# Kernel tuning notes

Hardware: AMD Instinct MI355X
Metric: run time of the kernel (lower is better)

Reference implementation:

```python
import jax, jax.numpy as jnp
import numpy as np

V, S, D, H, DK, DV, DFF, L, B, PAD = 32000, 2048, 512, 8, 64, 64, 2048, 2, 2, 0


def _pos_encoding(s, d):
    pos = jnp.arange(s, dtype=jnp.float32)[:, None]
    idx = jnp.arange(d // 2, dtype=jnp.float32)
    ang = pos / (10000.0 ** (2.0 * idx / d))  # [s, d/2]
    pe = jnp.zeros((s, d), jnp.float32)
    pe = pe.at[:, 0::2].set(jnp.sin(ang))
    pe = pe.at[:, 1::2].set(jnp.cos(ang))
    return pe


def _stable_softmax(x):
    # matches torch: max clamped to >= 0, denom + 1e-9 (all -inf row -> zeros)
    m = jnp.clip(jnp.max(x, axis=-1, keepdims=True), 0.0, None)
    e = jnp.exp(x - m)
    return e / (jnp.sum(e, axis=-1, keepdims=True) + 1e-9)


def _ln(x, s, b):
    mu = jnp.mean(x, axis=-1, keepdims=True)
    var = jnp.mean((x - mu) ** 2, axis=-1, keepdims=True)
    return (x - mu) / jnp.sqrt(var + 1e-5) * s + b


def setup_inputs() -> dict:
    key = jax.random.key(0)
    ks = jax.random.split(key, 16)
    sc = 0.02
    emb = sc * jax.random.normal(ks[1], (V, D), jnp.float32)
    emb = emb.at[PAD].set(0.0)  # padding_idx row is zero
    return {
        'x': jax.random.randint(ks[0], (B, S), 0, V),
        'padding_mask': jnp.zeros((B, S), bool),
        'emb': emb,
        'wq': sc * jax.random.normal(ks[2], (L, D, H * DK), jnp.float32),
        'wk': sc * jax.random.normal(ks[3], (L, D, H * DK), jnp.float32),
        'wv': sc * jax.random.normal(ks[4], (L, D, H * DV), jnp.float32),
        'wo': sc * jax.random.normal(ks[5], (L, H * DV, D), jnp.float32),
        'ln1_s': jnp.ones((L, D), jnp.float32),
        'ln1_b': jnp.zeros((L, D), jnp.float32),
        'ln2_s': jnp.ones((L, D), jnp.float32),
        'ln2_b': jnp.zeros((L, D), jnp.float32),
        'w1': sc * jax.random.normal(ks[6], (L, D, DFF), jnp.float32),
        'b1': jnp.zeros((L, DFF), jnp.float32),
        'w2': sc * jax.random.normal(ks[7], (L, DFF, D), jnp.float32),
        'b2': jnp.zeros((L, D), jnp.float32),
        'w_out': sc * jax.random.normal(ks[8], (D, V), jnp.float32),
    }


def _forward(x, padding_mask, emb, wq, wk, wv, wo, ln1_s, ln1_b, ln2_s, ln2_b, w1, b1, w2, b2, w_out):
    b, s = x.shape
    pe = _pos_encoding(s, D)[None]  # [1, s, D]
    pe = jnp.where(padding_mask[:, :, None], 0.0, pe)  # zero PE at padding tokens
    h = emb[x] + pe  # [b, s, D]
    # causal mask INCLUDES the diagonal (torch.triu default), union with padding rows/cols
    causal = jnp.triu(jnp.ones((s, s), bool))
    mask = causal[None, None] | padding_mask[:, None, None, :] | padding_mask[:, None, :, None]
    for l in range(L):
        q = (h @ wq[l]).reshape(b, s, H, DK).transpose(0, 2, 1, 3)
        k = (h @ wk[l]).reshape(b, s, H, DK).transpose(0, 2, 1, 3)
        v = (h @ wv[l]).reshape(b, s, H, DV).transpose(0, 2, 1, 3)
        scores = jnp.einsum('bhqd,bhkd->bhqk', q, k) / jnp.sqrt(jnp.float32(DK))
        scores = jnp.where(mask, -jnp.inf, scores)
        attn = _stable_softmax(scores)  # [b, H, s, s]
        o = jnp.einsum('bhqk,bhkd->bhqd', attn, v)
        o = o.transpose(0, 2, 1, 3).reshape(b, s, H * DV) @ wo[l]
        h = _ln(h + o, ln1_s[l], ln1_b[l])  # post-LN residual
        ff = jax.nn.gelu(h @ w1[l] + b1[l], approximate=False) @ w2[l] + b2[l]
        h = _ln(h + ff, ln2_s[l], ln2_b[l])
    return h @ w_out  # logits [b, s, V]


def reference(x, padding_mask, emb, wq, wk, wv, wo, ln1_s, ln1_b, ln2_s, ln2_b, w1, b1, w2, b2, w_out):
    return _forward(x, padding_mask, emb, wq, wk, wv, wo, ln1_s, ln1_b, ln2_s, ln2_b, w1, b1, w2, b2, w_out)
```

## Files before the change

kernel.cpp:

```cpp
#include <hip/hip_runtime.h>
#include <hip/hip_bf16.h>
#include <stdint.h>

#define VOCAB  32000
#define SLEN   2048
#define DMODEL 512
#define NHEAD  8
#define HDIM   64
#define DFFN   2048
#define NLAYER 2
#define BATCH  2
#define NTOK   (BATCH*SLEN)

typedef unsigned short u16;
using short8 = __attribute__((ext_vector_type(8))) short;
using f32x4  = __attribute__((ext_vector_type(4))) float;
using ushort4v = __attribute__((ext_vector_type(4))) unsigned short;

__device__ __forceinline__ u16 f2bf(float f) {
  union { float f; uint32_t i; } v; v.f = f;
  uint32_t r = v.i + 0x7fffu + ((v.i >> 16) & 1u);
  return (u16)(r >> 16);
}

__device__ __forceinline__ void gload_lds16(const void* g, void* l) {
  __builtin_amdgcn_global_load_lds(
      (const __attribute__((address_space(1))) unsigned int*)g,
      (__attribute__((address_space(3))) unsigned int*)l,
      16, 0, 0);
}

__device__ __forceinline__ void tr_tile(const float* __restrict__ in, u16* __restrict__ out,
                                        int K, int N, int nb, int kb, int tid) {
  __shared__ float t[32][33];
  int tx = tid & 31, ty = tid >> 5;
  #pragma unroll
  for (int i = 0; i < 32; i += 8)
    t[ty + i][tx] = in[(size_t)(kb + ty + i) * N + nb + tx];
  __syncthreads();
  #pragma unroll
  for (int i = 0; i < 32; i += 8)
    out[(size_t)(nb + ty + i) * K + kb + tx] = f2bf(t[tx][ty + i]);
}

__global__ void transpose_qkvo(const float* __restrict__ wq, const float* __restrict__ wk,
                               const float* __restrict__ wv, const float* __restrict__ wo,
                               u16* __restrict__ qkvT, u16* __restrict__ woT) {
  int job = blockIdx.y;
  int l = job >> 2, which = job & 3;
  const float* in = (which == 0) ? wq : (which == 1) ? wk : (which == 2) ? wv : wo;
  in += (size_t)l * DMODEL * DMODEL;
  u16* out = (which < 3) ? qkvT + (size_t)l * 1536 * DMODEL + (size_t)which * DMODEL * DMODEL
                         : woT + (size_t)l * DMODEL * DMODEL;
  int tile = blockIdx.x;
  tr_tile(in, out, DMODEL, DMODEL, (tile & 15) * 32, (tile >> 4) * 32, threadIdx.x);
}

__global__ void transpose_ffn(const float* __restrict__ w1, const float* __restrict__ w2,
                              u16* __restrict__ w1T, u16* __restrict__ w2T) {
  int job = blockIdx.y;
  int l = job >> 1, which = job & 1;
  const float* in;
  u16* out;
  int K, N;
  if (which == 0) { in = w1 + (size_t)l * DMODEL * DFFN; out = w1T + (size_t)l * DFFN * DMODEL; K = DMODEL; N = DFFN; }
  else            { in = w2 + (size_t)l * DFFN * DMODEL; out = w2T + (size_t)l * DMODEL * DFFN; K = DFFN; N = DMODEL; }
  int tile = blockIdx.x;
  int ntx = N / 32;
  tr_tile(in, out, K, N, (tile % ntx) * 32, (tile / ntx) * 32, threadIdx.x);
}

__global__ void transpose_wout_kmaj(const float* __restrict__ in, u16* __restrict__ out) {
  const int nb = blockIdx.x, kt = blockIdx.y;
  const int t = threadIdx.x;
  u16* dst = out + ((size_t)(nb * 8 + kt)) * 16384;
  #pragma unroll
  for (int kg = 0; kg < 8; ++kg) {
    short8 v;
    #pragma unroll
    for (int e = 0; e < 8; ++e)
      v[e] = (short)f2bf(in[(size_t)(kt * 64 + kg * 8 + e) * VOCAB + nb * 256 + t]);
    *(short8*)(dst + (kg * 256 + t) * 8) = v;
  }
}

__global__ void embed_pe(const int* __restrict__ x, const float* __restrict__ emb,
                         float* __restrict__ hf, u16* __restrict__ hb) {
  int tok = blockIdx.x;
  int s = tok & (SLEN - 1);
  int d = threadIdx.x << 2;
  int t = x[tok];
  float4 ev = *(const float4*)(emb + (size_t)t * DMODEL + d);
  float pos = (float)s;
  const float cexp = -0.03597789207803197f;
  float i0 = (float)(d >> 1);
  float a0 = pos * expf(cexp * i0);
  float a1 = pos * expf(cexp * (i0 + 1.0f));
  float h0 = ev.x + sinf(a0);
  float h1 = ev.y + cosf(a0);
  float h2 = ev.z + sinf(a1);
  float h3 = ev.w + cosf(a1);
  size_t o = (size_t)tok * DMODEL + d;
  *(float4*)(hf + o) = make_float4(h0, h1, h2, h3);
  hb[o + 0] = f2bf(h0); hb[o + 1] = f2bf(h1);
  hb[o + 2] = f2bf(h2); hb[o + 3] = f2bf(h3);
}

template<int EPI, bool XCDS, int BM, int BN>
__global__ __launch_bounds__(256, 2)
void gemm_nt(const u16* __restrict__ A, const u16* __restrict__ Bt,
             float* __restrict__ Cf, u16* __restrict__ Cb, u16* __restrict__ Vt,
             const float* __restrict__ bias, int M, int N, int K) {
  constexpr int MI = BM / 32;
  constexpr int NI = BN / 32;
  __shared__ u16 As[BM * 64];
  __shared__ u16 Bs[BN * 64];
  const int tid = threadIdx.x;
  const int lane = tid & 63;
  const int lr = lane & 15, lg = lane >> 4;
  const int w = tid >> 6;

  int bx = blockIdx.x, by = blockIdx.y;
  if constexpr (XCDS) {
    int nwg = gridDim.x * gridDim.y;
    int bid = by * gridDim.x + bx;
    int cpx = nwg >> 3;
    bid = (bid & 7) * cpx + (bid >> 3);
    bx = bid % gridDim.x; by = bid / gridDim.x;
  }
  const int m0 = by * BM;
  const int n0 = bx * BN;
  const int wm = (w >> 1) * (BM / 2);
  const int wn = (w & 1) * (BN / 2);

  f32x4 acc[MI][NI] = {};

  for (int kt = 0; kt < K; kt += 64) {
    #pragma unroll
    for (int r = 0; r < BM / 32; ++r) {
      int chunk = r * 256 + tid;
      int row = chunk >> 3, ce = (chunk & 7) * 8;
      gload_lds16(A + (size_t)(m0 + row) * K + kt + ce, As + chunk * 8);
    }
    #pragma unroll
    for (int r = 0; r < BN / 32; ++r) {
      int chunk = r * 256 + tid;
      int row = chunk >> 3, ce = (chunk & 7) * 8;
      gload_lds16(Bt + (size_t)(n0 + row) * K + kt + ce, Bs + chunk * 8);
    }
    __syncthreads();
    #pragma unroll
    for (int ks = 0; ks < 2; ++ks) {
      short8 af[MI], bfr[NI];
      #pragma unroll
      for (int mi = 0; mi < MI; ++mi)
        af[mi] = *(const short8*)(As + (wm + mi * 16 + lr) * 64 + ks * 32 + lg * 8);
      #pragma unroll
      for (int ni = 0; ni < NI; ++ni)
        bfr[ni] = *(const short8*)(Bs + (wn + ni * 16 + lr) * 64 + ks * 32 + lg * 8);
      #pragma unroll
      for (int mi = 0; mi < MI; ++mi)
        #pragma unroll
        for (int ni = 0; ni < NI; ++ni)
          acc[mi][ni] = __builtin_amdgcn_mfma_f32_16x16x32_bf16(af[mi], bfr[ni], acc[mi][ni], 0, 0, 0);
    }
    __syncthreads();
  }

  #pragma unroll
  for (int mi = 0; mi < MI; ++mi)
    #pragma unroll
    for (int ni = 0; ni < NI; ++ni) {
      const int col = n0 + wn + ni * 16 + lr;
      const int row0 = m0 + wm + mi * 16 + lg * 4;
      float bv = 0.f;
      if constexpr (EPI == 3) bv = bias[col];
      if constexpr (EPI == 2) {
        if (col >= 1024) {
          int hd = col - 1024, hh = hd >> 6, d = hd & 63;
          int b2 = row0 >> 11, s = row0 & (SLEN - 1);
          int c2 = (s >> 3) & 15, e2 = s & 7;
          int cs2 = c2 ^ (d & 7);
          ushort4v pk;
          #pragma unroll
          for (int j = 0; j < 4; ++j) pk[j] = f2bf(acc[mi][ni][j]);
          size_t va = ((size_t)((b2 * NHEAD + hh) * HDIM + d) << 11) + (s & ~127) + cs2 * 8 + e2;
          *(ushort4v*)(Vt + va) = pk;
          continue;
        }
      }
      #pragma unroll
      for (int j = 0; j < 4; ++j) {
        const int row = row0 + j;
        float v = acc[mi][ni][j];
        if constexpr (EPI == 0) {
          Cf[(size_t)row * N + col] = v;
        } else if constexpr (EPI == 2) {
          int dh = col & 63;
          int cs = (col & ~63) | ((((dh >> 3) ^ (row & 7)) << 3) | (dh & 7));
          Cb[(size_t)row * N + cs] = f2bf(v);
        } else {
          float xb = v + bv;
          Cb[(size_t)row * N + col] = f2bf(0.5f * xb * (1.0f + erff(xb * 0.7071067811865476f)));
        }
      }
    }
}

template<int EPI, bool XCDS>
__global__ __launch_bounds__(512, 2)
void gemm_ring(const u16* __restrict__ A, const u16* __restrict__ Bt,
               float* __restrict__ Cf, u16* __restrict__ Cb,
               const float* __restrict__ bias, int M, int N, int K) {
  __shared__ u16 lds[3 * 24576];
  const int tid = threadIdx.x;
  const int lane = tid & 63;
  const int lr = lane & 15, lg = lane >> 4;
  const int w = tid >> 6;
  const int wm = (w >> 1) * 64;
  const int wn = (w & 1) * 64;
  const int sx8 = (lr & 7) << 3;

  int bx = blockIdx.x, by = blockIdx.y;
  if constexpr (XCDS) {
    int nwg = gridDim.x * gridDim.y;
    int bid = by * gridDim.x + bx;
    int cpx = nwg >> 3;
    bid = (bid & 7) * cpx + (bid >> 3);
    bx = bid % gridDim.x; by = bid / gridDim.x;
  }
  const int m0 = by * 256, n0 = bx * 128;
  const int NT = K >> 6;

  auto stage = [&](int slot, int t) {
    u16* ab = lds + slot * 24576;
    const u16* Ag = A + (size_t)m0 * K + t * 64;
    #pragma unroll
    for (int i = 0; i < 4; ++i) {
      int cl = i * 512 + tid;
      int row = cl >> 3, c = cl & 7;
      gload_lds16(Ag + (size_t)row * K + ((c ^ (row & 7)) << 3), ab + cl * 8);
    }
    u16* bb = ab + 16384;
    const u16* Bg = Bt + (size_t)n0 * K + t * 64;
    #pragma unroll
    for (int i = 0; i < 2; ++i) {
      int cl = i * 512 + tid;
      int row = cl >> 3, c = cl & 7;
      gload_lds16(Bg + (size_t)row * K + ((c ^ (row & 7)) << 3), bb + cl * 8);
    }
  };

  f32x4 acc[4][4] = {};
  stage(0, 0); stage(1, 1); stage(2, 2);

  for (int t = 0; t < NT; ++t) {
    const u16* ab = lds + (t % 3) * 24576;
    const u16* bb = ab + 16384;
    if (t < NT - 2)       asm volatile("s_waitcnt vmcnt(12)" ::: "memory");
    else if (t == NT - 2) asm volatile("s_waitcnt vmcnt(6)" ::: "memory");
    else                  asm volatile("s_waitcnt vmcnt(0)" ::: "memory");
    __builtin_amdgcn_s_barrier();
    __builtin_amdgcn_sched_barrier(0);

    short8 af0[4], bfr[8];
    #pragma unroll
    for (int mi = 0; mi < 2; ++mi)
      #pragma unroll
      for (int kk = 0; kk < 2; ++kk)
        af0[mi * 2 + kk] = *(const short8*)(ab + (wm + mi * 16 + lr) * 64 + ((((kk << 2) + lg) << 3) ^ sx8));
    #pragma unroll
    for (int ni = 0; ni < 4; ++ni)
      #pragma unroll
      for (int kk = 0; kk < 2; ++kk)
        bfr[ni * 2 + kk] = *(const short8*)(bb + (wn + ni * 16 + lr) * 64 + ((((kk << 2) + lg) << 3) ^ sx8));
    asm volatile("s_waitcnt lgkmcnt(0)" ::: "memory");
    __builtin_amdgcn_sched_barrier(0);
    __builtin_amdgcn_s_setprio(1);
    #pragma unroll
    for (int mi = 0; mi < 2; ++mi)
      #pragma unroll
      for (int ni = 0; ni < 4; ++ni)
        #pragma unroll
        for (int kk = 0; kk < 2; ++kk)
          acc[mi][ni] = __builtin_amdgcn_mfma_f32_16x16x32_bf16(af0[mi * 2 + kk], bfr[ni * 2 + kk], acc[mi][ni], 0, 0, 0);
    __builtin_amdgcn_s_setprio(0);

    short8 af1[4];
    #pragma unroll
    for (int mi = 0; mi < 2; ++mi)
      #pragma unroll
      for (int kk = 0; kk < 2; ++kk)
        af1[mi * 2 + kk] = *(const short8*)(ab + (wm + (mi + 2) * 16 + lr) * 64 + ((((kk << 2) + lg) << 3) ^ sx8));
    asm volatile("s_waitcnt lgkmcnt(0)" ::: "memory");
    __builtin_amdgcn_sched_barrier(0);
    __builtin_amdgcn_s_setprio(1);
    #pragma unroll
    for (int mi = 0; mi < 2; ++mi)
      #pragma unroll
      for (int ni = 0; ni < 4; ++ni)
        #pragma unroll
        for (int kk = 0; kk < 2; ++kk)
          acc[mi + 2][ni] = __builtin_amdgcn_mfma_f32_16x16x32_bf16(af1[mi * 2 + kk], bfr[ni * 2 + kk], acc[mi + 2][ni], 0, 0, 0);
    __builtin_amdgcn_s_setprio(0);
    __builtin_amdgcn_s_barrier();
    __builtin_amdgcn_sched_barrier(0);
    if (t + 3 < NT) stage(t % 3, t + 3);
  }

  #pragma unroll
  for (int mi = 0; mi < 4; ++mi)
    #pragma unroll
    for (int ni = 0; ni < 4; ++ni) {
      const int col = n0 + wn + ni * 16 + lr;
      float bv = 0.f;
      if constexpr (EPI == 3) bv = bias[col];
      #pragma unroll
      for (int j = 0; j < 4; ++j) {
        const int row = m0 + wm + mi * 16 + lg * 4 + j;
        float v = acc[mi][ni][j];
        if constexpr (EPI == 0) {
          Cf[(size_t)row * N + col] = v;
        } else {
          float xb = v + bv;
          Cb[(size_t)row * N + col] = f2bf(0.5f * xb * (1.0f + erff(xb * 0.7071067811865476f)));
        }
      }
    }
}

__global__ __launch_bounds__(512, 2)
void gemm8(const u16* __restrict__ A, const u16* __restrict__ Bkt,
           float* __restrict__ Cf, int M, int N, int K) {
  __shared__ u16 lds[65536];
  const int tid = threadIdx.x;
  const int lane = tid & 63;
  const int lr = lane & 15, lg = lane >> 4;
  const int w = tid >> 6;
  const int wm = (w >> 2) * 64;
  const int wn = (w & 3) * 64;
  const int sx8 = (lr & 7) << 3;

  const int nwg = gridDim.x * gridDim.y;
  const int bid = blockIdx.y * gridDim.x + blockIdx.x;
  const int g  = (bid & 7) * (nwg >> 3) + (bid >> 3);
  const int bx = g / (int)gridDim.y;
  const int by = g % (int)gridDim.y;
  const int m0 = by * 256, n0 = bx * 256;
  const int NT = K >> 6;

  auto stageA = [&](int t, int mh) {
    u16* dst = lds + (t & 1) * 32768 + mh * 8192;
    const u16* src = A + (size_t)(m0 + mh * 128) * K + t * 64;
    #pragma unroll
    for (int i = 0; i < 2; ++i) {
      int c = i * 512 + tid;
      int row = c >> 3, cc = c & 7;
      gload_lds16(src + (size_t)row * K + ((cc ^ (row & 7)) << 3), dst + c * 8);
    }
  };
  auto stageB = [&](int t, int kk) {
    u16* dst = lds + (t & 1) * 32768 + 16384 + kk * 8192;
    const u16* src = Bkt + ((size_t)bx * NT + t) * 16384 + kk * 8192;
    #pragma unroll
    for (int i = 0; i < 2; ++i) {
      int c = i * 512 + tid;
      gload_lds16(src + c * 8, dst + c * 8);
    }
  };

  f32x4 accL[4][4] = {};
  f32x4 accH[4][4] = {};

  stageA(0, 0); stageA(0, 1); stageB(0, 0); stageB(0, 1);

  for (int t = 0; t < NT; ++t) {
    const int ct = t & 1;
    const u16* Ab = lds + ct * 32768;
    const u16* Bb = Ab + 16384;
    const bool pf = (t + 1 < NT);

    asm volatile("s_waitcnt vmcnt(2)" ::: "memory");
    __builtin_amdgcn_s_barrier();
    __builtin_amdgcn_sched_barrier(0);
    short8 af[4], bf0[4], bf1[4];
    #pragma unroll
    for (int f = 0; f < 4; ++f)
      af[f] = *(const short8*)(Ab + (wm + f * 16 + lr) * 64 + ((lg << 3) ^ sx8));
    #pragma unroll
    for (int ni = 0; ni < 4; ++ni)
      bf0[ni] = *(const short8*)(Bb + (lg * 256 + wn + ni * 16 + lr) * 8);
    if (pf) stageA(t + 1, 0);
    __builtin_amdgcn_sched_barrier(0);
    __builtin_amdgcn_s_setprio(1);
    #pragma unroll
    for (int f = 0; f < 4; ++f)
      #pragma unroll
      for (int ni = 0; ni < 4; ++ni)
        accL[f][ni] = __builtin_amdgcn_mfma_f32_16x16x32_bf16(af[f], bf0[ni], accL[f][ni], 0, 0, 0);
    __builtin_amdgcn_s_setprio(0);

    #pragma unroll
    for (int f = 0; f < 4; ++f)
      af[f] = *(const short8*)(Ab + 8192 + (wm + f * 16 + lr) * 64 + ((lg << 3) ^ sx8));
    if (pf) stageA(t + 1, 1);
    __builtin_amdgcn_sched_barrier(0);
    __builtin_amdgcn_s_setprio(1);
    #pragma unroll
    for (int f = 0; f < 4; ++f)
      #pragma unroll
      for (int ni = 0; ni < 4; ++ni)
        accH[f][ni] = __builtin_amdgcn_mfma_f32_16x16x32_bf16(af[f], bf0[ni], accH[f][ni], 0, 0, 0);
    __builtin_amdgcn_s_setprio(0);

    if (pf) { asm volatile("s_waitcnt vmcnt(4)" ::: "memory"); }
    else    { asm volatile("s_waitcnt vmcnt(0)" ::: "memory"); }
    __builtin_amdgcn_s_barrier();
    __builtin_amdgcn_sched_barrier(0);
    #pragma unroll
    for (int f = 0; f < 4; ++f)
      af[f] = *(const short8*)(Ab + (wm + f * 16 + lr) * 64 + ((((4 + lg) << 3)) ^ sx8));
    #pragma unroll
    for (int ni = 0; ni < 4; ++ni)
      bf1[ni] = *(const short8*)(Bb + 8192 + (lg * 256 + wn + ni * 16 + lr) * 8);
    if (pf) stageB(t + 1, 0);
    __builtin_amdgcn_sched_barrier(0);
    __builtin_amdgcn_s_setprio(1);
    #pragma unroll
    for (int f = 0; f < 4; ++f)
      #pragma unroll
      for (int ni = 0; ni < 4; ++ni)
        accL[f][ni] = __builtin_amdgcn_mfma_f32_16x16x32_bf16(af[f], bf1[ni], accL[f][ni], 0, 0, 0);
    __builtin_amdgcn_s_setprio(0);

    #pragma unroll
    for (int f = 0; f < 4; ++f)
      af[f] = *(const short8*)(Ab + 8192 + (wm + f * 16 + lr) * 64 + ((((4 + lg) << 3)) ^ sx8));
    if (pf) stageB(t + 1, 1);
    __builtin_amdgcn_sched_barrier(0);
    __builtin_amdgcn_s_setprio(1);
    #pragma unroll
    for (int f = 0; f < 4; ++f)
      #pragma unroll
      for (int ni = 0; ni < 4; ++ni)
        accH[f][ni] = __builtin_amdgcn_mfma_f32_16x16x32_bf16(af[f], bf1[ni], accH[f][ni], 0, 0, 0);
    __builtin_amdgcn_s_setprio(0);
  }

  #pragma unroll
  for (int mh = 0; mh < 2; ++mh)
    #pragma unroll
    for (int f = 0; f < 4; ++f)
      #pragma unroll
      for (int ni = 0; ni < 4; ++ni) {
        const int col = n0 + wn + ni * 16 + lr;
        const int row0 = m0 + mh * 128 + wm + f * 16 + lg * 4;
        #pragma unroll
        for (int j = 0; j < 4; ++j) {
          float v = mh ? accH[f][ni][j] : accL[f][ni][j];
          __builtin_nontemporal_store(v, &Cf[(size_t)(row0 + j) * N + col]);
        }
      }
}

__global__ __launch_bounds__(256, 2)
void flash_attn(const u16* __restrict__ qkv, const u16* __restrict__ vT,
                u16* __restrict__ Og) {
  const int bid = blockIdx.x;
  const int qt = (bid < 256) ? (31 - (bid >> 4)) : ((bid - 256) >> 4);
  const int hb = bid & 15;
  const int h  = hb & 7;
  const int b  = hb >> 3;
  const int tid = threadIdx.x;
  const int lane = tid & 63;
  const int w = tid >> 6;
  const int lr = lane & 15, lg = lane >> 4;
  const int sx = lr & 7;

  __shared__ u16 Ks[128 * 64];
  __shared__ u16 Vs[64 * 128];
  __shared__ u16 Pl[4][16 * 132];

  const u16* Qb = qkv + (size_t)(b * SLEN + qt * 64) * 1536 + h * 64;
  const u16* Kb = qkv + (size_t)(b * SLEN) * 1536 + 512 + h * 64;
  const u16* Vb = vT + ((size_t)(b * NHEAD + h) * HDIM) * SLEN;

  #pragma unroll
  for (int r = 0; r < 2; ++r) {
    int chunk = r * 256 + tid;
    int row = chunk >> 3, cc = chunk & 7;
    gload_lds16(Qb + (size_t)row * 1536 + cc * 8, Ks + chunk * 8);
  }
  __syncthreads();
  short8 qf[2];
  #pragma unroll
  for (int ks = 0; ks < 2; ++ks)
    qf[ks] = *(const short8*)(Ks + (w * 16 + lr) * 64 + ((((ks << 2) + lg) ^ sx) << 3));
  __syncthreads();

  f32x4 mrow = {};
  f32x4 lrow = {};
  f32x4 accO[4] = {};
  const float SC = 0.18033688011112042f;

  const int ktmax = (qt * 64 + 62) >> 7;
  for (int kt = 0; kt <= ktmax; ++kt) {
    #pragma unroll
    for (int r = 0; r < 4; ++r) {
      int chunk = r * 256 + tid;
      int row = chunk >> 3, cc = chunk & 7;
      gload_lds16(Kb + (size_t)(kt * 128 + row) * 1536 + cc * 8, Ks + chunk * 8);
    }
    #pragma unroll
    for (int r = 0; r < 4; ++r) {
      int chunk = r * 256 + tid;
      int drow = chunk >> 4, cc = chunk & 15;
      gload_lds16(Vb + (size_t)drow * SLEN + kt * 128 + cc * 8, Vs + chunk * 8);
    }
    __syncthreads();

    f32x4 sfr[8];
    #pragma unroll
    for (int ni = 0; ni < 8; ++ni) {
      f32x4 a = {};
      #pragma unroll
      for (int ks = 0; ks < 2; ++ks) {
        short8 kf = *(const short8*)(Ks + (ni * 16 + lr) * 64 + ((((ks << 2) + lg) ^ sx) << 3));
        a = __builtin_amdgcn_mfma_f32_16x16x32_bf16(qf[ks], kf, a, 0, 0, 0);
      }
      sfr[ni] = a * SC;
    }
    if (kt == ktmax) {
      #pragma unroll
      for (int ni = 0; ni < 8; ++ni)
        #pragma unroll
        for (int j = 0; j < 4; ++j) {
          int kg = kt * 128 + ni * 16 + lr;
          int qg = qt * 64 + w * 16 + lg * 4 + j;
          if (kg >= qg) sfr[ni][j] = -1e30f;
        }
    }
    f32x4 tmax = sfr[0];
    #pragma unroll
    for (int ni = 1; ni < 8; ++ni)
      #pragma unroll
      for (int j = 0; j < 4; ++j) tmax[j] = fmaxf(tmax[j], sfr[ni][j]);
    #pragma unroll
    for (int off = 1; off < 16; off <<= 1)
      #pragma unroll
      for (int j = 0; j < 4; ++j) tmax[j] = fmaxf(tmax[j], __shfl_xor(tmax[j], off));
    f32x4 mnew, scl;
    #pragma unroll
    for (int j = 0; j < 4; ++j) {
      mnew[j] = fmaxf(mrow[j], tmax[j]);
      scl[j]  = exp2f(mrow[j] - mnew[j]);
    }
    f32x4 rsum = {};
    #pragma unroll
    for (int ni = 0; ni < 8; ++ni)
      #pragma unroll
      for (int j = 0; j < 4; ++j) {
        float pv = exp2f(sfr[ni][j] - mnew[j]);
        sfr[ni][j] = pv;
        rsum[j] += pv;
      }
    #pragma unroll
    for (int off = 1; off < 16; off <<= 1)
      #pragma unroll
      for (int j = 0; j < 4; ++j) rsum[j] += __shfl_xor(rsum[j], off);
    #pragma unroll
    for (int j = 0; j < 4; ++j) { lrow[j] = lrow[j] * scl[j] + rsum[j]; mrow[j] = mnew[j]; }
    #pragma unroll
    for (int di = 0; di < 4; ++di)
      #pragma unroll
      for (int j = 0; j < 4; ++j) accO[di][j] *= scl[j];

    u16* pw = Pl[w];
    #pragma unroll
    for (int ni = 0; ni < 8; ++ni)
      #pragma unroll
      for (int j = 0; j < 4; ++j)
        pw[(lg * 4 + j) * 132 + ni * 16 + lr] = f2bf(sfr[ni][j]);

    asm volatile("s_waitcnt lgkmcnt(0)" ::: "memory");

    #pragma unroll
    for (int ks = 0; ks < 4; ++ks) {
      short8 pa = *(const short8*)(pw + lr * 132 + ks * 32 + lg * 8);
      #pragma unroll
      for (int di = 0; di < 4; ++di) {
        short8 vbf = *(const short8*)(Vs + (di * 16 + lr) * 128 + ((((ks << 2) + lg) ^ sx) << 3));
        accO[di] = __builtin_amdgcn_mfma_f32_16x16x32_bf16(pa, vbf, accO[di], 0, 0, 0);
      }
    }
    __syncthreads();
  }

  u16* Ob = Og + ((size_t)(b * SLEN + qt * 64 + w * 16)) * DMODEL + h * HDIM;
  f32x4 inv;
  #pragma unroll
  for (int j = 0; j < 4; ++j) inv[j] = 1.0f / (lrow[j] + 1e-9f);
  #pragma unroll
  for (int di = 0; di < 4; ++di)
    #pragma unroll
    for (int j = 0; j < 4; ++j)
      Ob[(size_t)(lg * 4 + j) * DMODEL + di * 16 + lr] = f2bf(accO[di][j] * inv[j]);
}

__global__ void ln_res(const float* __restrict__ hin, const float* __restrict__ yin,
                       const float* __restrict__ badd,
                       const float* __restrict__ sc, const float* __restrict__ bi,
                       float* __restrict__ hout, u16* __restrict__ hb) {
  int row = blockIdx.x * 4 + (threadIdx.x >> 6);
  int lane = threadIdx.x & 63;
  size_t base = (size_t)row * DMODEL;
  float v[8];
  float sum = 0.f;
  #pragma unroll
  for (int i = 0; i < 8; ++i) {
    int d = lane * 8 + i;
    float t = hin[base + d] + yin[base + d];
    if (badd) t += badd[d];
    v[i] = t; sum += t;
  }
  #pragma unroll
  for (int off = 1; off < 64; off <<= 1) sum += __shfl_xor(sum, off);
  float mu = sum * (1.f / 512.f);
  float sq = 0.f;
  #pragma unroll
  for (int i = 0; i < 8; ++i) { float dv = v[i] - mu; sq += dv * dv; }
  #pragma unroll
  for (int off = 1; off < 64; off <<= 1) sq += __shfl_xor(sq, off);
  float rstd = rsqrtf(sq * (1.f / 512.f) + 1e-5f);
  #pragma unroll
  for (int i = 0; i < 8; ++i) {
    int d = lane * 8 + i;
    float o = (v[i] - mu) * rstd * sc[d] + bi[d];
    hout[base + d] = o;
    hb[base + d] = f2bf(o);
  }
}

extern "C" void kernel_launch(void* const* d_in, const int* in_sizes, int n_in,
                              void* d_out, int out_size, void* d_ws, size_t ws_size,
                              hipStream_t stream) {
  (void)in_sizes; (void)n_in; (void)out_size; (void)ws_size;
  const int*   x    = (const int*)d_in[0];
  const float* emb  = (const float*)d_in[2];
  const float* wq   = (const float*)d_in[3];
  const float* wk   = (const float*)d_in[4];
  const float* wv   = (const float*)d_in[5];
  const float* wo   = (const float*)d_in[6];
  const float* ln1s = (const float*)d_in[7];
  const float* ln1b = (const float*)d_in[8];
  const float* ln2s = (const float*)d_in[9];
  const float* ln2b = (const float*)d_in[10];
  const float* w1   = (const float*)d_in[11];
  const float* b1   = (const float*)d_in[12];
  const float* w2   = (const float*)d_in[13];
  const float* b2   = (const float*)d_in[14];
  const float* wout = (const float*)d_in[15];

  char* p = (char*)d_ws;
  auto alloc = [&](size_t bytes) { char* q = p; p += (bytes + 255) & ~(size_t)255; return q; };
  float* hf    = (float*)alloc((size_t)NTOK * DMODEL * 4);
  u16*  hb     = (u16*) alloc((size_t)NTOK * DMODEL * 2);
  u16*  qkvb   = (u16*) alloc((size_t)NTOK * 1536 * 2);
  u16*  vTb    = (u16*) alloc((size_t)NTOK * DMODEL * 2);
  u16*  obuf   = (u16*) alloc((size_t)NTOK * DMODEL * 2);
  float* y32   = (float*)alloc((size_t)NTOK * DMODEL * 4);
  u16*  ff1g   = (u16*) alloc((size_t)NTOK * DFFN * 2);
  u16*  wqkvT  = (u16*) alloc((size_t)NLAYER * 1536 * DMODEL * 2);
  u16*  woT    = (u16*) alloc((size_t)NLAYER * DMODEL * DMODEL * 2);
  u16*  w1T    = (u16*) alloc((size_t)NLAYER * DMODEL * DFFN * 2);
  u16*  w2T    = (u16*) alloc((size_t)NLAYER * DFFN * DMODEL * 2);
  u16*  woutK  = (u16*) alloc((size_t)VOCAB * DMODEL * 2);

  transpose_qkvo<<<dim3(256, 8), 256, 0, stream>>>(wq, wk, wv, wo, wqkvT, woT);
  transpose_ffn<<<dim3(1024, 4), 256, 0, stream>>>(w1, w2, w1T, w2T);
  transpose_wout_kmaj<<<dim3(VOCAB / 256, DMODEL / 64), 256, 0, stream>>>(wout, woutK);

  embed_pe<<<NTOK, 128, 0, stream>>>(x, emb, hf, hb);

  for (int l = 0; l < NLAYER; ++l) {
    size_t o = (size_t)l * DMODEL * DMODEL;
    gemm_nt<2, false, 128, 128><<<dim3(12, 32), 256, 0, stream>>>(
        hb, wqkvT + (size_t)l * 1536 * DMODEL, nullptr, qkvb, vTb, nullptr, NTOK, 1536, DMODEL);
    flash_attn<<<dim3(512), 256, 0, stream>>>(qkvb, vTb, obuf);
    gemm_nt<0, false, 64, 128><<<dim3(4, 64), 256, 0, stream>>>(
        obuf, woT + o, y32, nullptr, nullptr, nullptr, NTOK, DMODEL, DMODEL);
    ln_res<<<NTOK / 4, 256, 0, stream>>>(hf, y32, nullptr, ln1s + l * DMODEL, ln1b + l * DMODEL, hf, hb);
    gemm_ring<3, false><<<dim3(DFFN / 128, NTOK / 256), 512, 0, stream>>>(
        hb, w1T + (size_t)l * DFFN * DMODEL, nullptr, ff1g, b1 + l * DFFN, NTOK, DFFN, DMODEL);
    gemm_nt<0, false, 64, 128><<<dim3(4, 64), 256, 0, stream>>>(
        ff1g, w2T + (size_t)l * DMODEL * DFFN, y32, nullptr, nullptr, nullptr, NTOK, DMODEL, DFFN);
    ln_res<<<NTOK / 4, 256, 0, stream>>>(hf, y32, b2 + l * DMODEL, ln2s + l * DMODEL, ln2b + l * DMODEL, hf, hb);
  }
  gemm8<<<dim3(VOCAB / 256, NTOK / 256), 512, 0, stream>>>(
      hb, woutK, (float*)d_out, NTOK, VOCAB, DMODEL);
}
```

Measured before the change: 572.0 us.

## Use 32x32x16 MFMA in vocab GEMM and merge weight transpose kernels

```diff
diff --git a/kernel.cpp b/kernel.cpp
--- a/kernel.cpp
+++ b/kernel.cpp
@@ -15,6 +15,7 @@
 typedef unsigned short u16;
 using short8 = __attribute__((ext_vector_type(8))) short;
 using f32x4  = __attribute__((ext_vector_type(4))) float;
+using f32x16 = __attribute__((ext_vector_type(16))) float;
 using ushort4v = __attribute__((ext_vector_type(4))) unsigned short;
 
 __device__ __forceinline__ u16 f2bf(float f) {
@@ -30,9 +31,9 @@
       16, 0, 0);
 }
 
-__device__ __forceinline__ void tr_tile(const float* __restrict__ in, u16* __restrict__ out,
+__device__ __forceinline__ void tr_tile(float (*t)[33],
+                                        const float* __restrict__ in, u16* __restrict__ out,
                                         int K, int N, int nb, int kb, int tid) {
-  __shared__ float t[32][33];
   int tx = tid & 31, ty = tid >> 5;
   #pragma unroll
   for (int i = 0; i < 32; i += 8)
@@ -43,44 +44,45 @@
     out[(size_t)(nb + ty + i) * K + kb + tx] = f2bf(t[tx][ty + i]);
 }
 
-__global__ void transpose_qkvo(const float* __restrict__ wq, const float* __restrict__ wk,
-                               const float* __restrict__ wv, const float* __restrict__ wo,
-                               u16* __restrict__ qkvT, u16* __restrict__ woT) {
-  int job = blockIdx.y;
-  int l = job >> 2, which = job & 3;
-  const float* in = (which == 0) ? wq : (which == 1) ? wk : (which == 2) ? wv : wo;
-  in += (size_t)l * DMODEL * DMODEL;
-  u16* out = (which < 3) ? qkvT + (size_t)l * 1536 * DMODEL + (size_t)which * DMODEL * DMODEL
-                         : woT + (size_t)l * DMODEL * DMODEL;
-  int tile = blockIdx.x;
-  tr_tile(in, out, DMODEL, DMODEL, (tile & 15) * 32, (tile >> 4) * 32, threadIdx.x);
-}
-
-__global__ void transpose_ffn(const float* __restrict__ w1, const float* __restrict__ w2,
-                              u16* __restrict__ w1T, u16* __restrict__ w2T) {
-  int job = blockIdx.y;
-  int l = job >> 1, which = job & 1;
-  const float* in;
-  u16* out;
-  int K, N;
-  if (which == 0) { in = w1 + (size_t)l * DMODEL * DFFN; out = w1T + (size_t)l * DFFN * DMODEL; K = DMODEL; N = DFFN; }
-  else            { in = w2 + (size_t)l * DFFN * DMODEL; out = w2T + (size_t)l * DMODEL * DFFN; K = DFFN; N = DMODEL; }
-  int tile = blockIdx.x;
-  int ntx = N / 32;
-  tr_tile(in, out, K, N, (tile % ntx) * 32, (tile / ntx) * 32, threadIdx.x);
-}
-
-__global__ void transpose_wout_kmaj(const float* __restrict__ in, u16* __restrict__ out) {
-  const int nb = blockIdx.x, kt = blockIdx.y;
-  const int t = threadIdx.x;
-  u16* dst = out + ((size_t)(nb * 8 + kt)) * 16384;
-  #pragma unroll
-  for (int kg = 0; kg < 8; ++kg) {
-    short8 v;
-    #pragma unroll
-    for (int e = 0; e < 8; ++e)
-      v[e] = (short)f2bf(in[(size_t)(kt * 64 + kg * 8 + e) * VOCAB + nb * 256 + t]);
-    *(short8*)(dst + (kg * 256 + t) * 8) = v;
+__global__ void transpose_all(const float* __restrict__ wq, const float* __restrict__ wk,
+                              const float* __restrict__ wv, const float* __restrict__ wo,
+                              const float* __restrict__ w1, const float* __restrict__ w2,
+                              const float* __restrict__ wout,
+                              u16* __restrict__ qkvT, u16* __restrict__ woT,
+                              u16* __restrict__ w1T, u16* __restrict__ w2T,
+                              u16* __restrict__ woutK) {
+  __shared__ float t[32][33];
+  const int bid = blockIdx.x;
+  const int tid = threadIdx.x;
+  if (bid < 2048) {
+    int job = bid >> 8, tile = bid & 255;
+    int l = job >> 2, which = job & 3;
+    const float* in = (which == 0) ? wq : (which == 1) ? wk : (which == 2) ? wv : wo;
+    in += (size_t)l * DMODEL * DMODEL;
+    u16* out = (which < 3) ? qkvT + (size_t)l * 1536 * DMODEL + (size_t)which * DMODEL * DMODEL
+                           : woT + (size_t)l * DMODEL * DMODEL;
+    tr_tile(t, in, out, DMODEL, DMODEL, (tile & 15) * 32, (tile >> 4) * 32, tid);
+  } else if (bid < 6144) {
+    int rel = bid - 2048;
+    int job = rel >> 10, tile = rel & 1023;
+    int l = job >> 1, which = job & 1;
+    const float* in; u16* out; int K, N;
+    if (which == 0) { in = w1 + (size_t)l * DMODEL * DFFN; out = w1T + (size_t)l * DFFN * DMODEL; K = DMODEL; N = DFFN; }
+    else            { in = w2 + (size_t)l * DFFN * DMODEL; out = w2T + (size_t)l * DMODEL * DFFN; K = DFFN; N = DMODEL; }
+    int ntx = N / 32;
+    tr_tile(t, in, out, K, N, (tile % ntx) * 32, (tile / ntx) * 32, tid);
+  } else {
+    int rel = bid - 6144;
+    int nb = rel >> 3, kt = rel & 7;
+    u16* dst = woutK + ((size_t)(nb * 8 + kt)) * 16384;
+    #pragma unroll
+    for (int kg = 0; kg < 8; ++kg) {
+      short8 v;
+      #pragma unroll
+      for (int e = 0; e < 8; ++e)
+        v[e] = (short)f2bf(wout[(size_t)(kt * 64 + kg * 8 + e) * VOCAB + nb * 256 + tid]);
+      *(short8*)(dst + (kg * 256 + tid) * 8) = v;
+    }
   }
 }
 
@@ -335,12 +337,11 @@
   __shared__ u16 lds[65536];
   const int tid = threadIdx.x;
   const int lane = tid & 63;
-  const int lr = lane & 15, lg = lane >> 4;
+  const int l31 = lane & 31, l5 = lane >> 5;
+  const int rx = lane & 7;
   const int w = tid >> 6;
   const int wm = (w >> 2) * 64;
   const int wn = (w & 3) * 64;
-  const int sx8 = (lr & 7) << 3;
-
   const int nwg = gridDim.x * gridDim.y;
   const int bid = blockIdx.y * gridDim.x + blockIdx.x;
   const int g  = (bid & 7) * (nwg >> 3) + (bid >> 3);
@@ -369,48 +370,57 @@
     }
   };
 
-  f32x4 accL[4][4] = {};
-  f32x4 accH[4][4] = {};
+  f32x16 accL[2][2] = {};
+  f32x16 accH[2][2] = {};
 
   stageA(0, 0); stageA(0, 1); stageB(0, 0); stageB(0, 1);
 
   for (int t = 0; t < NT; ++t) {
-    const int ct = t & 1;
-    const u16* Ab = lds + ct * 32768;
+    const u16* Ab = lds + (t & 1) * 32768;
     const u16* Bb = Ab + 16384;
     const bool pf = (t + 1 < NT);
+    short8 af[4], b0[4], b1[4];
 
     asm volatile("s_waitcnt vmcnt(2)" ::: "memory");
     __builtin_amdgcn_s_barrier();
     __builtin_amdgcn_sched_barrier(0);
-    short8 af[4], bf0[4], bf1[4];
-    #pragma unroll
-    for (int f = 0; f < 4; ++f)
-      af[f] = *(const short8*)(Ab + (wm + f * 16 + lr) * 64 + ((lg << 3) ^ sx8));
-    #pragma unroll
-    for (int ni = 0; ni < 4; ++ni)
-      bf0[ni] = *(const short8*)(Bb + (lg * 256 + wn + ni * 16 + lr) * 8);
+    #pragma unroll
+    for (int mf = 0; mf < 2; ++mf)
+      #pragma unroll
+      for (int ks = 0; ks < 2; ++ks)
+        af[mf * 2 + ks] = *(const short8*)(Ab + (wm + mf * 32 + l31) * 64 + (((ks * 2 + l5) ^ rx) << 3));
+    #pragma unroll
+    for (int nf = 0; nf < 2; ++nf)
+      #pragma unroll
+      for (int ks = 0; ks < 2; ++ks)
+        b0[nf * 2 + ks] = *(const short8*)(Bb + ((ks * 2 + l5) * 256 + wn + nf * 32 + l31) * 8);
     if (pf) stageA(t + 1, 0);
     __builtin_amdgcn_sched_barrier(0);
     __builtin_amdgcn_s_setprio(1);
     #pragma unroll
-    for (int f = 0; f < 4; ++f)
-      #pragma unroll
-      for (int ni = 0; ni < 4; ++ni)
-        accL[f][ni] = __builtin_amdgcn_mfma_f32_16x16x32_bf16(af[f], bf0[ni], accL[f][ni], 0, 0, 0);
+    for (int ks = 0; ks < 2; ++ks)
+      #pragma unroll
+      for (int mf = 0; mf < 2; ++mf)
+        #pragma unroll
+        for (int nf = 0; nf < 2; ++nf)
+          accL[mf][nf] = __builtin_amdgcn_mfma_f32_32x32x16_bf16(af[mf * 2 + ks], b0[nf * 2 + ks], accL[mf][nf], 0, 0, 0);
     __builtin_amdgcn_s_setprio(0);
 
     #pragma unroll
-    for (int f = 0; f < 4; ++f)
-      af[f] = *(const short8*)(Ab + 8192 + (wm + f * 16 + lr) * 64 + ((lg << 3) ^ sx8));
+    for (int mf = 0; mf < 2; ++mf)
+      #pragma unroll
+      for (int ks = 0; ks < 2; ++ks)
+        af[mf * 2 + ks] = *(const short8*)(Ab + 8192 + (wm + mf * 32 + l31) * 64 + (((ks * 2 + l5) ^ rx) << 3));
     if (pf) stageA(t + 1, 1);
     __builtin_amdgcn_sched_barrier(0);
     __builtin_amdgcn_s_setprio(1);
     #pragma unroll
-    for (int f = 0; f < 4; ++f)
-      #pragma unroll
-      for (int ni = 0; ni < 4; ++ni)
-        accH[f][ni] = __builtin_amdgcn_mfma_f32_16x16x32_bf16(af[f], bf0[ni], accH[f][ni], 0, 0, 0);
+    for (int ks = 0; ks < 2; ++ks)
+      #pragma unroll
+      for (int mf = 0; mf < 2; ++mf)
+        #pragma unroll
+        for (int nf = 0; nf < 2; ++nf)
+          accH[mf][nf] = __builtin_amdgcn_mfma_f32_32x32x16_bf16(af[mf * 2 + ks], b0[nf * 2 + ks], accH[mf][nf], 0, 0, 0);
     __builtin_amdgcn_s_setprio(0);
 
     if (pf) { asm volatile("s_waitcnt vmcnt(4)" ::: "memory"); }
@@ -418,47 +428,58 @@
     __builtin_amdgcn_s_barrier();
     __builtin_amdgcn_sched_barrier(0);
     #pragma unroll
-    for (int f = 0; f < 4; ++f)
-      af[f] = *(const short8*)(Ab + (wm + f * 16 + lr) * 64 + ((((4 + lg) << 3)) ^ sx8));
-    #pragma unroll
-    for (int ni = 0; ni < 4; ++ni)
-      bf1[ni] = *(const short8*)(Bb + 8192 + (lg * 256 + wn + ni * 16 + lr) * 8);
+    for (int mf = 0; mf < 2; ++mf)
+      #pragma unroll
+      for (int ks = 0; ks < 2; ++ks)
+        af[mf * 2 + ks] = *(const short8*)(Ab + (wm + mf * 32 + l31) * 64 + (((4 + ks * 2 + l5) ^ rx) << 3));
+    #pragma unroll
+    for (int nf = 0; nf < 2; ++nf)
+      #pragma unroll
+      for (int ks = 0; ks < 2; ++ks)
+        b1[nf * 2 + ks] = *(const short8*)(Bb + ((4 + ks * 2 + l5) * 256 + wn + nf * 32 + l31) * 8);
     if (pf) stageB(t + 1, 0);
     __builtin_amdgcn_sched_barrier(0);
     __builtin_amdgcn_s_setprio(1);
     #pragma unroll
-    for (int f = 0; f < 4; ++f)
-      #pragma unroll
-      for (int ni = 0; ni < 4; ++ni)
-        accL[f][ni] = __builtin_amdgcn_mfma_f32_16x16x32_bf16(af[f], bf1[ni], accL[f][ni], 0, 0, 0);
+    for (int ks = 0; ks < 2; ++ks)
+      #pragma unroll
+      for (int mf = 0; mf < 2; ++mf)
+        #pragma unroll
+        for (int nf = 0; nf < 2; ++nf)
+          accL[mf][nf] = __builtin_amdgcn_mfma_f32_32x32x16_bf16(af[mf * 2 + ks], b1[nf * 2 + ks], accL[mf][nf], 0, 0, 0);
     __builtin_amdgcn_s_setprio(0);
 
     #pragma unroll
-    for (int f = 0; f < 4; ++f)
-      af[f] = *(const short8*)(Ab + 8192 + (wm + f * 16 + lr) * 64 + ((((4 + lg) << 3)) ^ sx8));
+    for (int mf = 0; mf < 2; ++mf)
+      #pragma unroll
+      for (int ks = 0; ks < 2; ++ks)
+        af[mf * 2 + ks] = *(const short8*)(Ab + 8192 + (wm + mf * 32 + l31) * 64 + (((4 + ks * 2 + l5) ^ rx) << 3));
     if (pf) stageB(t + 1, 1);
     __builtin_amdgcn_sched_barrier(0);
     __builtin_amdgcn_s_setprio(1);
     #pragma unroll
-    for (int f = 0; f < 4; ++f)
-      #pragma unroll
-      for (int ni = 0; ni < 4; ++ni)
-        accH[f][ni] = __builtin_amdgcn_mfma_f32_16x16x32_bf16(af[f], bf1[ni], accH[f][ni], 0, 0, 0);
+    for (int ks = 0; ks < 2; ++ks)
+      #pragma unroll
+      for (int mf = 0; mf < 2; ++mf)
+        #pragma unroll
+        for (int nf = 0; nf < 2; ++nf)
+          accH[mf][nf] = __builtin_amdgcn_mfma_f32_32x32x16_bf16(af[mf * 2 + ks], b1[nf * 2 + ks], accH[mf][nf], 0, 0, 0);
     __builtin_amdgcn_s_setprio(0);
   }
 
   #pragma unroll
   for (int mh = 0; mh < 2; ++mh)
     #pragma unroll
-    for (int f = 0; f < 4; ++f)
-      #pragma unroll
-      for (int ni = 0; ni < 4; ++ni) {
-        const int col = n0 + wn + ni * 16 + lr;
-        const int row0 = m0 + mh * 128 + wm + f * 16 + lg * 4;
-        #pragma unroll
-        for (int j = 0; j < 4; ++j) {
-          float v = mh ? accH[f][ni][j] : accL[f][ni][j];
-          __builtin_nontemporal_store(v, &Cf[(size_t)(row0 + j) * N + col]);
+    for (int mf = 0; mf < 2; ++mf)
+      #pragma unroll
+      for (int nf = 0; nf < 2; ++nf) {
+        const int col = n0 + wn + nf * 32 + l31;
+        const int rbase = m0 + mh * 128 + wm + mf * 32 + 4 * l5;
+        #pragma unroll
+        for (int reg = 0; reg < 16; ++reg) {
+          const int row = rbase + (reg & 3) + 8 * (reg >> 2);
+          float v = mh ? accH[mf][nf][reg] : accL[mf][nf][reg];
+          __builtin_nontemporal_store(v, &Cf[(size_t)row * N + col]);
         }
       }
 }
@@ -676,9 +697,8 @@
   u16*  w2T    = (u16*) alloc((size_t)NLAYER * DFFN * DMODEL * 2);
   u16*  woutK  = (u16*) alloc((size_t)VOCAB * DMODEL * 2);
 
-  transpose_qkvo<<<dim3(256, 8), 256, 0, stream>>>(wq, wk, wv, wo, wqkvT, woT);
-  transpose_ffn<<<dim3(1024, 4), 256, 0, stream>>>(w1, w2, w1T, w2T);
-  transpose_wout_kmaj<<<dim3(VOCAB / 256, DMODEL / 64), 256, 0, stream>>>(wout, woutK);
+  transpose_all<<<dim3(7144), 256, 0, stream>>>(wq, wk, wv, wo, w1, w2, wout,
+                                                wqkvT, woT, w1T, w2T, woutK);
 
   embed_pe<<<NTOK, 128, 0, stream>>>(x, emb, hf, hb);
 
```

Result: faster. 550.5 us (-3.8%).
